# Kernel optimization log

Hardware: AMD Instinct MI355X
Metric: run time of the kernel (lower is better)

Reference implementation:

```python
import jax, jax.numpy as jnp
import numpy as np

B, L, D, H = 1, 1024, 768, 12
h = D // H  # 64
EPS = 1e-5
ALPHA = 0.01  # leaky relu slope


def setup_inputs() -> dict:
    key = jax.random.key(0)
    ks = jax.random.split(key, 10)
    s = 0.02
    f32 = jnp.float32
    return {
        "x": jax.random.normal(ks[0], (B, L, D), f32),
        "filters": jax.random.normal(ks[1], (L, h), f32) * s,  # spectral filters [L, h]
        "wq_w": jax.random.normal(ks[2], (D, D), f32) * s,
        "wq_b": jnp.zeros((D,), f32),
        "wk_w": jax.random.normal(ks[3], (D, D), f32) * s,
        "wk_b": jnp.zeros((D,), f32),
        "wv_w": jax.random.normal(ks[4], (D, D), f32) * s,
        "wv_b": jnp.zeros((D,), f32),
        "wo_w": jax.random.normal(ks[5], (D, D), f32) * s,
        "wo_b": jnp.zeros((D,), f32),
        "wg_w": jax.random.normal(ks[6], (h * h, 1), f32) * s,
        "wg_b": jnp.zeros((1,), f32),
        "qk_scale": jnp.ones((1, H, 1), f32) + jax.random.normal(ks[7], (1, H, 1), f32) * 0.02,
        "kv_scale": jnp.ones((1, H, 1, 1, 1), f32) + jax.random.normal(ks[8], (1, H, 1, 1, 1), f32) * 0.02,
    }


def _causal_fft_conv(f, u):
    """Per-head-channel causal FFT convolution. f: [L,h], u: [B,H,L,h] -> [B,H,L,h]."""
    n = 2 * L  # >= L + L - 1 for linear (full) convolution
    Ff = jnp.fft.rfft(f, n=n, axis=0)            # [n//2+1, h]
    Uf = jnp.fft.rfft(u, n=n, axis=2)            # [B,H,n//2+1,h]
    y = jnp.fft.irfft(Uf * Ff[None, None], n=n, axis=2)
    return y[:, :, :L, :]


def _l2norm(t):
    # matches F.normalize(dim=-1): x / max(||x||, 1e-12)
    nrm = jnp.sqrt(jnp.sum(t * t, axis=-1, keepdims=True))
    return t / jnp.maximum(nrm, 1e-12)


def _combine(a, b):
    """Associative combine: (m, s, n, Z, g) running-max / exp-sum / exp-weighted-v / outer-product / gate-sum."""
    m_x, s_x, n_x, Z_x, g_x = a
    m_y, s_y, n_y, Z_y, g_y = b
    m = jnp.maximum(m_x, m_y)
    ex = jnp.exp(m_x - m)
    ey = jnp.exp(m_y - m)
    return (m,
            s_x * ex + s_y * ey,
            n_x * ex[..., None] + n_y * ey[..., None],
            Z_x + Z_y,
            g_x + g_y)


def reference(x, filters, wq_w, wq_b, wk_w, wk_b, wv_w, wv_b, wo_w, wo_b,
              wg_w, wg_b, qk_scale, kv_scale):
    # split heads: [B,H,L,h]
    bhld = x.reshape(B, L, H, h).transpose(0, 2, 1, 3)
    # spectral filtering (tensordot_conv): per-channel causal conv with filters
    xt = _causal_fft_conv(filters, bhld)                       # [B,H,L,h]
    xt = xt.transpose(0, 2, 1, 3).reshape(B, L, D)             # [B,L,D]

    q = (xt @ wq_w + wq_b).reshape(B, L, H, h).transpose(0, 2, 1, 3)
    k = (xt @ wk_w + wk_b).reshape(B, L, H, h).transpose(0, 2, 1, 3)
    v = (xt @ wv_w + wv_b).reshape(B, L, H, h).transpose(0, 2, 1, 3)
    q, k, v = _l2norm(q), _l2norm(k), _l2norm(v)

    sim = jnp.einsum('bhld,bhld->bhl', q, k) * qk_scale         # [B,H,L]
    # Z[b,h,s,p,n] = v[b,h,s,p] * k[b,h,s,n]
    Z = jnp.einsum('bhsn,bhsp->bhspn', k, v) * kv_scale         # [B,H,L,h,h]

    gate_logits = Z.reshape(B, H, L, h * h) @ wg_w + wg_b       # [B,H,L,1]
    gl = jnp.where(gate_logits > 0, gate_logits, ALPHA * gate_logits)
    gates = (gl * gl + EPS)[..., 0]                             # [B,H,L]
    gated_Z = Z * gates[..., None, None]

    leaves = (sim, jnp.ones_like(sim), v, gated_Z, gates)
    m_s, s_s, n_s, Z_s, g_s = jax.lax.associative_scan(_combine, leaves, axis=2)

    linear_attn = n_s / (s_s[..., None] + EPS)                  # [B,H,L,h]
    softmax_w = jnp.exp(sim - m_s) / (s_s + EPS)                # [B,H,L]
    Hm = Z_s / (g_s[..., None, None] + EPS)                     # [B,H,L,h,h]
    ctx = jnp.einsum('bhtp,bhtpn->bhtn', q, Hm)                 # [B,H,L,h]
    qla = linear_attn
    lerp = ctx + (qla - ctx) * softmax_w[..., None]

    y = lerp.transpose(0, 2, 1, 3).reshape(B, L, D)
    return y @ wo_w + wo_b
```

## Files before the change

kernel.cpp:

```cpp
#include <hip/hip_runtime.h>
#include <hip/hip_bf16.h>

constexpr int LS = 1024;
constexpr int DM = 768;
constexpr int NH = 12;
constexpr int HD = 64;
constexpr float EPSF = 1e-5f;
constexpr float ALPHAF = 0.01f;

constexpr int SG = 16;
constexpr int NTL = LS / SG;
constexpr int WSZ = DM * DM;
constexpr int NPAR = 8;

typedef unsigned short u16;
typedef __attribute__((ext_vector_type(8))) short bf16x8;
typedef __attribute__((ext_vector_type(8))) unsigned short u16x8;
typedef __attribute__((ext_vector_type(4))) float f32x4;

__device__ __forceinline__ u16 f2b(float f) {
  unsigned u = __float_as_uint(f);
  u += 0x7FFFu + ((u >> 16) & 1u);
  return (u16)(u >> 16);
}
__device__ __forceinline__ float b2f(u16 b) {
  return __uint_as_float((unsigned)b << 16);
}

__device__ __forceinline__ void gld16(const u16* g, void* l) {
  __builtin_amdgcn_global_load_lds(
      (const __attribute__((address_space(1))) void*)g,
      (__attribute__((address_space(3))) void*)l, 16, 0, 0);
}

__global__ __launch_bounds__(256) void conv_txw_kernel(
    const float* __restrict__ x, const float* __restrict__ f,
    const float* __restrict__ wq, const float* __restrict__ wk,
    const float* __restrict__ wv, const float* __restrict__ wo,
    u16* __restrict__ wT, u16* __restrict__ pbase) {
  extern __shared__ char smem[];
  const int b = blockIdx.x;
  const int tid = threadIdx.x;

  if (b >= 1536) {
    const int b2 = b - 1536;
    const int kb = (b2 % 12) * 64, nb = ((b2 / 12) % 12) * 64, z = b2 / 144;
    const float* src = (z == 0) ? wq : (z == 1) ? wk : (z == 2) ? wv : wo;
    u16* dst = wT + (size_t)z * WSZ;
    float (*T)[65] = (float(*)[65])smem;
#pragma unroll
    for (int rep = 0; rep < 4; ++rep) {
      const int r = rep * 16 + (tid >> 4);
      const int c4 = (tid & 15) * 4;
      const float4 v4 = *(const float4*)(src + (size_t)(kb + r) * DM + nb + c4);
      T[r][c4] = v4.x; T[r][c4 + 1] = v4.y; T[r][c4 + 2] = v4.z; T[r][c4 + 3] = v4.w;
    }
    __syncthreads();
#pragma unroll
    for (int rep = 0; rep < 4; ++rep) {
      const int n = rep * 16 + (tid >> 4);
      const int k4 = (tid & 15) * 4;
      ushort4 o;
      o.x = f2b(T[k4 + 0][n]); o.y = f2b(T[k4 + 1][n]);
      o.z = f2b(T[k4 + 2][n]); o.w = f2b(T[k4 + 3][n]);
      *(ushort4*)(dst + (size_t)(nb + n) * DM + kb + k4) = o;
    }
    return;
  }

  const int lcg  = b & 15;
  const int head = (b >> 4) % 12;
  const int par  = b / 192;
  const int lane = tid & 63;
  const int wid  = tid >> 6;
  const int lc   = lcg * 4 + wid;
  const int l0   = lc * 16;

  const float* xg = x + head * HD + lane;
  const float* fg = f + lane;

  float acc[16];
#pragma unroll
  for (int t = 0; t < 16; ++t) acc[t] = 0.f;

  for (int sc = par; sc <= lc; sc += NPAR) {
    const int s0 = sc * 16;
    const int d0 = l0 - s0 - 15;
    float xw[16], fr[31];
#pragma unroll
    for (int m = 0; m < 16; ++m) xw[m] = xg[(s0 + m) * DM];
    if (sc < lc) {
#pragma unroll
      for (int m = 0; m < 31; ++m) fr[m] = fg[(d0 + m) * HD];
    } else {
#pragma unroll
      for (int m = 0; m < 15; ++m) fr[m] = 0.f;
#pragma unroll
      for (int m = 15; m < 31; ++m) fr[m] = fg[(d0 + m) * HD];
    }
#pragma unroll
    for (int li = 0; li < 16; ++li)
#pragma unroll
      for (int si = 0; si < 16; ++si)
        acc[li] = fmaf(fr[li - si + 15], xw[si], acc[li]);
  }

  u16* __restrict__ xt_p = pbase + (size_t)par * LS * DM;
#pragma unroll
  for (int li = 0; li < 16; ++li)
    xt_p[(size_t)(l0 + li) * DM + head * HD + lane] = f2b(acc[li]);
}

__global__ __launch_bounds__(256) void pack_xt(const u16* __restrict__ pbase,
                                               u16* __restrict__ xtb) {
  const size_t NT = (size_t)LS * DM;
  const size_t i = ((size_t)blockIdx.x * 256 + threadIdx.x) * 8;
  float s[8] = {};
#pragma unroll
  for (int p = 0; p < NPAR; ++p) {
    const u16x8 v8 = *(const u16x8*)(pbase + p * NT + i);
#pragma unroll
    for (int e = 0; e < 8; ++e) s[e] += b2f(v8[e]);
  }
  u16x8 o;
#pragma unroll
  for (int e = 0; e < 8; ++e) o[e] = f2b(s[e]);
  *(u16x8*)(xtb + i) = o;
}

__global__ __launch_bounds__(256) void qkv_mfma(const u16* __restrict__ xtb,
                                                const u16* __restrict__ wT,
                                                const float* __restrict__ bq,
                                                const float* __restrict__ bk,
                                                const float* __restrict__ bv,
                                                float* __restrict__ qo,
                                                float* __restrict__ ko,
                                                float* __restrict__ vo) {
  const int b = blockIdx.x;
  const int xcd = b & 7, j = b >> 3;
  const int rt = (xcd & 3) * 4 + j / 6;
  const int ct = (xcd >> 2) * 6 + j % 6;

  __shared__ u16 As[64 * 64];
  __shared__ u16 Bs[3][64 * 64];

  const int tid = threadIdx.x, w = tid >> 6, l = tid & 63;
  const int wr = w >> 1, wc = w & 1;

  const int srow1 = tid >> 3, sc16 = tid & 7;
  const int c16L1 = sc16 ^ (srow1 & 7);
  const int srow2 = srow1 + 32;
  const int c16L2 = sc16 ^ (srow2 & 7);

  const u16* Ag1 = xtb + (size_t)(rt * 64 + srow1) * DM + c16L1 * 8;
  const u16* Ag2 = xtb + (size_t)(rt * 64 + srow2) * DM + c16L2 * 8;

  char* lA = (char*)As + w * 1024;

  f32x4 acc[3][2][2] = {};
  for (int kb = 0; kb < DM; kb += 64) {
    gld16(Ag1 + kb, lA);
    gld16(Ag2 + kb, lA + 4096);
#pragma unroll
    for (int z = 0; z < 3; ++z) {
      const u16* wz = wT + (size_t)z * WSZ;
      const u16* Bg1 = wz + (size_t)(ct * 64 + srow1) * DM + c16L1 * 8;
      const u16* Bg2 = wz + (size_t)(ct * 64 + srow2) * DM + c16L2 * 8;
      char* lB = (char*)Bs[z] + w * 1024;
      gld16(Bg1 + kb, lB);
      gld16(Bg2 + kb, lB + 4096);
    }
    __syncthreads();
#pragma unroll
    for (int kk = 0; kk < 2; ++kk) {
      bf16x8 a[2];
#pragma unroll
      for (int ar = 0; ar < 2; ++ar) {
        const int row = wr * 32 + ar * 16 + (l & 15);
        const int c16 = ((kk << 2) + (l >> 4)) ^ (row & 7);
        a[ar] = *(const bf16x8*)((char*)As + row * 128 + c16 * 16);
      }
#pragma unroll
      for (int z = 0; z < 3; ++z) {
        bf16x8 bb[2];
#pragma unroll
        for (int bc = 0; bc < 2; ++bc) {
          const int col = wc * 32 + bc * 16 + (l & 15);
          const int c16 = ((kk << 2) + (l >> 4)) ^ (col & 7);
          bb[bc] = *(const bf16x8*)((char*)Bs[z] + col * 128 + c16 * 16);
        }
#pragma unroll
        for (int ar = 0; ar < 2; ++ar)
#pragma unroll
          for (int bc = 0; bc < 2; ++bc)
            acc[z][ar][bc] = __builtin_amdgcn_mfma_f32_16x16x32_bf16(
                a[ar], bb[bc], acc[z][ar][bc], 0, 0, 0);
      }
    }
    __syncthreads();
  }

  const float* biasArr[3] = {bq, bk, bv};
  float* outArr[3] = {qo, ko, vo};
  const int rbase = rt * 64 + wr * 32 + ((l >> 4) << 2);
  const int cb = wc * 32 + (l & 15);
#pragma unroll
  for (int z = 0; z < 3; ++z) {
    const float* bias = biasArr[z];
    float* out = outArr[z];
#pragma unroll
    for (int ar = 0; ar < 2; ++ar)
#pragma unroll
      for (int bc = 0; bc < 2; ++bc) {
        const int col = cb + bc * 16;
        const float bbv = bias[ct * 64 + col];
#pragma unroll
        for (int r = 0; r < 4; ++r)
          out[((size_t)ct * LS + rbase + ar * 16 + r) * HD + col] =
              acc[z][ar][bc][r] + bbv;
      }
  }
}

__global__ __launch_bounds__(256) void out_mfma(const u16* __restrict__ lerpb,
                                                const u16* __restrict__ woT,
                                                const float* __restrict__ bias,
                                                float* __restrict__ out) {
  const int b = blockIdx.x;
  const int xcd = b & 7, j = b >> 3;
  const int unit = xcd * 3 + (j >> 3), sub = j & 7;
  const int ct = unit >> 1, rt = (unit & 1) * 8 + sub;

  __shared__ u16 As[64 * 64];
  __shared__ u16 Bs[64 * 64];

  const int tid = threadIdx.x, w = tid >> 6, l = tid & 63;
  const int wr = w >> 1, wc = w & 1;

  const int srow1 = tid >> 3, sc16 = tid & 7;
  const int c16L1 = sc16 ^ (srow1 & 7);
  const int srow2 = srow1 + 32;
  const int c16L2 = sc16 ^ (srow2 & 7);

  const u16* Ag1 = lerpb + (size_t)(rt * 64 + srow1) * DM + c16L1 * 8;
  const u16* Ag2 = lerpb + (size_t)(rt * 64 + srow2) * DM + c16L2 * 8;
  const u16* Bg1 = woT + (size_t)(ct * 64 + srow1) * DM + c16L1 * 8;
  const u16* Bg2 = woT + (size_t)(ct * 64 + srow2) * DM + c16L2 * 8;

  char* lA = (char*)As + w * 1024;
  char* lB = (char*)Bs + w * 1024;

  f32x4 acc[2][2] = {};
  for (int kb = 0; kb < DM; kb += 64) {
    gld16(Ag1 + kb, lA);
    gld16(Ag2 + kb, lA + 4096);
    gld16(Bg1 + kb, lB);
    gld16(Bg2 + kb, lB + 4096);
    __syncthreads();
#pragma unroll
    for (int kk = 0; kk < 2; ++kk) {
      bf16x8 a[2], bb[2];
#pragma unroll
      for (int ar = 0; ar < 2; ++ar) {
        const int row = wr * 32 + ar * 16 + (l & 15);
        const int c16 = ((kk << 2) + (l >> 4)) ^ (row & 7);
        a[ar] = *(const bf16x8*)((char*)As + row * 128 + c16 * 16);
      }
#pragma unroll
      for (int bc = 0; bc < 2; ++bc) {
        const int col = wc * 32 + bc * 16 + (l & 15);
        const int c16 = ((kk << 2) + (l >> 4)) ^ (col & 7);
        bb[bc] = *(const bf16x8*)((char*)Bs + col * 128 + c16 * 16);
      }
#pragma unroll
      for (int ar = 0; ar < 2; ++ar)
#pragma unroll
        for (int bc = 0; bc < 2; ++bc)
          acc[ar][bc] = __builtin_amdgcn_mfma_f32_16x16x32_bf16(
              a[ar], bb[bc], acc[ar][bc], 0, 0, 0);
    }
    __syncthreads();
  }

  const int rbase = rt * 64 + wr * 32 + ((l >> 4) << 2);
  const int cb = wc * 32 + (l & 15);
#pragma unroll
  for (int ar = 0; ar < 2; ++ar)
#pragma unroll
    for (int bc = 0; bc < 2; ++bc) {
      const int col = ct * 64 + cb + bc * 16;
      const float bbv = bias[col];
#pragma unroll
      for (int r = 0; r < 4; ++r)
        out[(size_t)(rbase + ar * 16 + r) * DM + col] = acc[ar][bc][r] + bbv;
    }
}

__global__ __launch_bounds__(256) void nsg_state_kernel(
    float* __restrict__ q, float* __restrict__ k, float* __restrict__ v,
    const float* __restrict__ wg, const float* __restrict__ wgb,
    const float* __restrict__ qk_scale, const float* __restrict__ kv_scale,
    float* __restrict__ sim, float* __restrict__ gates,
    float* __restrict__ states, float* __restrict__ nes) {
  const int j = blockIdx.x, head = blockIdx.y;
  const int s0 = j * SG;
  const int tid = threadIdx.x;
  const int wid = tid >> 6, lane = tid & 63;
  __shared__ alignas(16) float Vs[SG][68];
  __shared__ alignas(16) float Kg[SG][68];
  __shared__ float Es[SG];

  auto red = [](float x) {
#pragma unroll
    for (int o = 32; o; o >>= 1) x += __shfl_xor(x, o);
    return x;
  };

  const float qks = qk_scale[head], kvs = kv_scale[head], wb = wgb[0];
#pragma unroll
  for (int it = 0; it < 4; ++it) {
    const int rr = wid * 4 + it;
    const size_t idx = ((size_t)head * LS + s0 + rr) * HD + lane;
    float qv = q[idx], kv = k[idx], vv = v[idx];
    const float qn = fmaxf(sqrtf(red(qv * qv)), 1e-12f);
    const float kn = fmaxf(sqrtf(red(kv * kv)), 1e-12f);
    const float vn = fmaxf(sqrtf(red(vv * vv)), 1e-12f);
    qv /= qn; kv /= kn; vv /= vn;
    q[idx] = qv; k[idx] = kv; v[idx] = vv;
    const float s = red(qv * kv) * qks;
    Vs[rr][lane] = vv;
    float t = 0.f;
#pragma unroll 8
    for (int p = 0; p < 64; ++p) t = fmaf(Vs[rr][p], wg[p * 64 + lane], t);
    float gl = red(t * kv) * kvs + wb;
    gl = gl > 0.f ? gl : ALPHAF * gl;
    const float g = gl * gl + EPSF;
    Kg[rr][lane] = kv * g;
    if (lane == 0) {
      sim[head * LS + s0 + rr] = s;
      gates[head * LS + s0 + rr] = g;
      Es[rr] = expf(s);
    }
  }
  __syncthreads();

  const int p0 = (tid >> 4) * 4, n0 = (tid & 15) * 4;
  float acc[4][4] = {};
  for (int s = 0; s < SG; ++s) {
    const float4 ra = *(const float4*)&Vs[s][p0];
    const float4 rb = *(const float4*)&Kg[s][n0];
    const float av[4] = {ra.x, ra.y, ra.z, ra.w};
    const float bv[4] = {rb.x, rb.y, rb.z, rb.w};
#pragma unroll
    for (int i = 0; i < 4; ++i)
#pragma unroll
      for (int jj = 0; jj < 4; ++jj)
        acc[i][jj] = fmaf(av[i], bv[jj], acc[i][jj]);
  }
  float* Sout = states + (size_t)(head * NTL + j) * 4096;
#pragma unroll
  for (int i = 0; i < 4; ++i)
    *(float4*)&Sout[(p0 + i) * 64 + n0] =
        make_float4(acc[i][0], acc[i][1], acc[i][2], acc[i][3]);

  if (tid < HD) {
    float ne = 0.f;
#pragma unroll
    for (int s = 0; s < SG; ++s) ne = fmaf(Es[s], Vs[s][tid], ne);
    nes[(size_t)(head * NTL + j) * HD + tid] = ne;
  }
}

__global__ __launch_bounds__(1024) void scan_prefix_kernel(
    const float* __restrict__ sim, const float* __restrict__ gates,
    float* __restrict__ m_s, float* __restrict__ Sraw, float* __restrict__ g_s,
    float* __restrict__ states, float* __restrict__ nes) {
  const int head = blockIdx.x, chunk = blockIdx.y;
  const int tid = threadIdx.x, lane = tid & 63, wid = tid >> 6;

  if (chunk == 0) {
    __shared__ float wm[16], wS[16], wg2[16];
    const float sv = sim[head * LS + tid];
    float m = sv, S = expf(sv), g = gates[head * LS + tid];
#pragma unroll
    for (int off = 1; off < 64; off <<= 1) {
      const float pm = __shfl_up(m, off);
      const float pS = __shfl_up(S, off);
      const float pg = __shfl_up(g, off);
      if (lane >= off) { m = fmaxf(m, pm); S += pS; g += pg; }
    }
    if (lane == 63) { wm[wid] = m; wS[wid] = S; wg2[wid] = g; }
    __syncthreads();
    for (int w2 = 0; w2 < wid; ++w2) {
      m = fmaxf(m, wm[w2]); S += wS[w2]; g += wg2[w2];
    }
    m_s[head * LS + tid] = m;
    Sraw[head * LS + tid] = S;
    g_s[head * LS + tid] = g;

    if (tid < HD) {
      float a = 0.f;
      float* nb = nes + (size_t)head * NTL * HD + tid;
#pragma unroll 4
      for (int jj = 0; jj < NTL; ++jj) {
        float* p = nb + (size_t)jj * HD;
        const float t = *p;
        *p = a;
        a += t;
      }
    }
  }

  {
    float a = 0.f;
    float* base = states + (size_t)head * NTL * 4096 + chunk * 1024 + tid;
#pragma unroll 4
    for (int jj = 0; jj < NTL; ++jj) {
      float* p = base + (size_t)jj * 4096;
      const float t = *p;
      *p = a;
      a += t;
    }
  }
}

__global__ __launch_bounds__(256) void apply_kernel(const float* __restrict__ q,
                                                    const float* __restrict__ k,
                                                    const float* __restrict__ v,
                                                    const float* __restrict__ sim,
                                                    const float* __restrict__ gates,
                                                    const float* __restrict__ m_s,
                                                    const float* __restrict__ Sraw,
                                                    const float* __restrict__ g_s,
                                                    const float* __restrict__ states,
                                                    const float* __restrict__ nes,
                                                    const float* __restrict__ kv_scale,
                                                    u16* __restrict__ lerpb) {
  const int bt = blockIdx.x, head = blockIdx.y;
  const int t0 = bt * SG;
  const int tid = threadIdx.x;
  __shared__ alignas(16) float Ps[64][68];
  __shared__ alignas(16) float Qs[SG][68];
  __shared__ alignas(16) float Vs[SG][68];
  __shared__ alignas(16) float Ks[SG][68];
  __shared__ alignas(16) float NEp[64];
  __shared__ float Ag[SG][SG + 1];
  __shared__ float Es[SG], Gs[SG];

  const float* Pg = states + (size_t)(head * NTL + bt) * 4096;
#pragma unroll
  for (int rep = 0; rep < 4; ++rep) {
    const int lin = rep * 1024 + tid * 4;
    *(float4*)&Ps[lin >> 6][lin & 63] = *(const float4*)(Pg + lin);
  }
  {
    const int r = tid >> 4, c = (tid & 15) * 4;
    const size_t rowbase = ((size_t)head * LS + t0 + r) * HD;
    *(float4*)&Qs[r][c] = *(const float4*)(q + rowbase + c);
    *(float4*)&Ks[r][c] = *(const float4*)(k + rowbase + c);
    *(float4*)&Vs[r][c] = *(const float4*)(v + rowbase + c);
  }
  if (tid < SG) {
    Es[tid] = expf(sim[head * LS + t0 + tid]);
    Gs[tid] = gates[head * LS + t0 + tid];
  }
  if (tid < HD) NEp[tid] = nes[(size_t)(head * NTL + bt) * HD + tid];
  __syncthreads();

  {
    const int t = tid >> 4, s = tid & 15;
    float a = 0.f;
    if (s <= t) {
#pragma unroll
      for (int p = 0; p < 64; p += 4) {
        const float4 q4 = *(const float4*)&Qs[t][p];
        const float4 v4 = *(const float4*)&Vs[s][p];
        a = fmaf(q4.x, v4.x, a); a = fmaf(q4.y, v4.y, a);
        a = fmaf(q4.z, v4.z, a); a = fmaf(q4.w, v4.w, a);
      }
      a *= Gs[s];
    }
    Ag[t][s] = a;
  }
  __syncthreads();

  const int r = tid >> 4, c0 = (tid & 15) * 4;
  float4 O = make_float4(0.f, 0.f, 0.f, 0.f);
#pragma unroll 8
  for (int p = 0; p < 64; ++p) {
    const float qv = Qs[r][p];
    const float4 p4 = *(const float4*)&Ps[p][c0];
    O.x = fmaf(qv, p4.x, O.x); O.y = fmaf(qv, p4.y, O.y);
    O.z = fmaf(qv, p4.z, O.z); O.w = fmaf(qv, p4.w, O.w);
  }
  float4 Nn = *(const float4*)&NEp[c0];
  for (int s = 0; s <= r; ++s) {
    const float ag = Ag[r][s];
    const float es = Es[s];
    const float4 k4 = *(const float4*)&Ks[s][c0];
    const float4 v4 = *(const float4*)&Vs[s][c0];
    O.x = fmaf(ag, k4.x, O.x); O.y = fmaf(ag, k4.y, O.y);
    O.z = fmaf(ag, k4.z, O.z); O.w = fmaf(ag, k4.w, O.w);
    Nn.x = fmaf(es, v4.x, Nn.x); Nn.y = fmaf(es, v4.y, Nn.y);
    Nn.z = fmaf(es, v4.z, Nn.z); Nn.w = fmaf(es, v4.w, Nn.w);
  }

  const int t = t0 + r;
  const float m  = m_s[head * LS + t];
  const float em = expf(-m);
  const float ss = Sraw[head * LS + t] * em;
  const float inv = 1.f / (ss + EPSF);
  const float sw  = expf(sim[head * LS + t] - m) * inv;
  const float gi  = kv_scale[head] / (g_s[head * LS + t] + EPSF);
  const float ei  = em * inv;
  float rx, ry, rz, rw;
  { const float cx = O.x * gi, la = Nn.x * ei; rx = cx + (la - cx) * sw; }
  { const float cx = O.y * gi, la = Nn.y * ei; ry = cx + (la - cx) * sw; }
  { const float cx = O.z * gi, la = Nn.z * ei; rz = cx + (la - cx) * sw; }
  { const float cx = O.w * gi, la = Nn.w * ei; rw = cx + (la - cx) * sw; }
  ushort4 ob;
  ob.x = f2b(rx); ob.y = f2b(ry); ob.z = f2b(rz); ob.w = f2b(rw);
  *(ushort4*)&lerpb[(size_t)t * DM + head * HD + c0] = ob;
}

extern "C" void kernel_launch(void* const* d_in, const int* in_sizes, int n_in,
                              void* d_out, int out_size, void* d_ws, size_t ws_size,
                              hipStream_t stream) {
  (void)in_sizes; (void)n_in; (void)out_size; (void)ws_size;
  const float* x        = (const float*)d_in[0];
  const float* filters  = (const float*)d_in[1];
  const float* wq_w     = (const float*)d_in[2];
  const float* wq_b     = (const float*)d_in[3];
  const float* wk_w     = (const float*)d_in[4];
  const float* wk_b     = (const float*)d_in[5];
  const float* wv_w     = (const float*)d_in[6];
  const float* wv_b     = (const float*)d_in[7];
  const float* wo_w     = (const float*)d_in[8];
  const float* wo_b     = (const float*)d_in[9];
  const float* wg_w     = (const float*)d_in[10];
  const float* wg_b     = (const float*)d_in[11];
  const float* qk_scale = (const float*)d_in[12];
  const float* kv_scale = (const float*)d_in[13];

  float* ws = (float*)d_ws;
  const size_t NT = (size_t)LS * DM;
  float* q     = ws;
  float* k     = ws + NT;
  float* v     = ws + 2 * NT;
  float* sim   = ws + 3 * NT;
  float* gates = sim + NH * LS;
  float* m_s   = gates + NH * LS;
  float* Sraw  = m_s + NH * LS;
  float* g_s   = Sraw + NH * LS;
  float* states = g_s + NH * LS;
  float* nes    = states + (size_t)NH * NTL * 4096;
  u16*   xtb    = (u16*)(nes + (size_t)NH * NTL * HD);
  u16*   wT     = xtb + NT;
  u16*   lerpb  = wT + 4 * (size_t)WSZ;
  u16*   pbase  = lerpb + NT;

  conv_txw_kernel<<<dim3(2112), 256, 16640, stream>>>(
      x, filters, wq_w, wk_w, wv_w, wo_w, wT, pbase);
  pack_xt<<<dim3(NT / 2048), 256, 0, stream>>>(pbase, xtb);
  qkv_mfma<<<dim3(192), 256, 0, stream>>>(xtb, wT, wq_b, wk_b, wv_b, q, k, v);
  nsg_state_kernel<<<dim3(NTL, NH), 256, 0, stream>>>(
      q, k, v, wg_w, wg_b, qk_scale, kv_scale, sim, gates, states, nes);
  scan_prefix_kernel<<<dim3(NH, 4), 1024, 0, stream>>>(
      sim, gates, m_s, Sraw, g_s, states, nes);
  apply_kernel<<<dim3(NTL, NH), 256, 0, stream>>>(
      q, k, v, sim, gates, m_s, Sraw, g_s, states, nes, kv_scale, lerpb);
  out_mfma<<<dim3(192), 256, 0, stream>>>(
      lerpb, wT + 3 * (size_t)WSZ, wo_b, (float*)d_out);
}
```

Baseline: 103.1 us.

## Transpose x and filters into channel-major layout before causal convolution

A prep kernel now transposes x to [head*channel, L] and the filters to a zero-padded channel-major buffer, alongside the existing weight transpose to bf16. The convolution kernel then reads contiguous float4 vectors per lane instead of one strided scalar per row, and the padding removes the diagonal-tile branch. This trades an extra kernel launch and an extra pass over x through memory for fewer scattered loads in the convolution's inner loop. It also separates the weight transpose from the convolution launch, so the two no longer share one grid.

```diff
diff --git a/kernel.cpp b/kernel.cpp
--- a/kernel.cpp
+++ b/kernel.cpp
@@ -12,6 +12,7 @@
 constexpr int NTL = LS / SG;
 constexpr int WSZ = DM * DM;
 constexpr int NPAR = 8;
+constexpr int FTS = 1056;
 
 typedef unsigned short u16;
 typedef __attribute__((ext_vector_type(8))) short bf16x8;
@@ -33,41 +34,97 @@
       (__attribute__((address_space(3))) void*)l, 16, 0, 0);
 }
 
-__global__ __launch_bounds__(256) void conv_txw_kernel(
+__global__ __launch_bounds__(256) void prep_kernel(
     const float* __restrict__ x, const float* __restrict__ f,
     const float* __restrict__ wq, const float* __restrict__ wk,
     const float* __restrict__ wv, const float* __restrict__ wo,
-    u16* __restrict__ wT, u16* __restrict__ pbase) {
-  extern __shared__ char smem[];
+    u16* __restrict__ wT, float* __restrict__ xT, float* __restrict__ fT) {
+  __shared__ float T[64][65];
   const int b = blockIdx.x;
   const int tid = threadIdx.x;
 
-  if (b >= 1536) {
-    const int b2 = b - 1536;
-    const int kb = (b2 % 12) * 64, nb = ((b2 / 12) % 12) * 64, z = b2 / 144;
-    const float* src = (z == 0) ? wq : (z == 1) ? wk : (z == 2) ? wv : wo;
-    u16* dst = wT + (size_t)z * WSZ;
-    float (*T)[65] = (float(*)[65])smem;
+  if (b < 192) {
+    const int head = b / 16, l0 = (b % 16) * 64;
+    const int r = tid >> 2, c4 = (tid & 3) * 16;
 #pragma unroll
     for (int rep = 0; rep < 4; ++rep) {
-      const int r = rep * 16 + (tid >> 4);
-      const int c4 = (tid & 15) * 4;
-      const float4 v4 = *(const float4*)(src + (size_t)(kb + r) * DM + nb + c4);
-      T[r][c4] = v4.x; T[r][c4 + 1] = v4.y; T[r][c4 + 2] = v4.z; T[r][c4 + 3] = v4.w;
+      const int c = c4 + rep * 4;
+      const float4 v4 = *(const float4*)(x + (size_t)(l0 + r) * DM + head * HD + c);
+      T[r][c] = v4.x; T[r][c + 1] = v4.y; T[r][c + 2] = v4.z; T[r][c + 3] = v4.w;
     }
     __syncthreads();
+    const int ch = tid >> 2, l4 = (tid & 3) * 16;
+    float* dst = xT + ((size_t)head * HD + ch) * LS + l0;
 #pragma unroll
     for (int rep = 0; rep < 4; ++rep) {
-      const int n = rep * 16 + (tid >> 4);
-      const int k4 = (tid & 15) * 4;
-      ushort4 o;
-      o.x = f2b(T[k4 + 0][n]); o.y = f2b(T[k4 + 1][n]);
-      o.z = f2b(T[k4 + 2][n]); o.w = f2b(T[k4 + 3][n]);
-      *(ushort4*)(dst + (size_t)(nb + n) * DM + kb + k4) = o;
+      const int li = l4 + rep * 4;
+      float4 v4;
+      v4.x = T[li + 0][ch]; v4.y = T[li + 1][ch];
+      v4.z = T[li + 2][ch]; v4.w = T[li + 3][ch];
+      *(float4*)(dst + li) = v4;
     }
     return;
   }
-
+  if (b < 208) {
+    const int d0 = (b - 192) * 64;
+    const int r = tid >> 2, c4 = (tid & 3) * 16;
+#pragma unroll
+    for (int rep = 0; rep < 4; ++rep) {
+      const int c = c4 + rep * 4;
+      const float4 v4 = *(const float4*)(f + (size_t)(d0 + r) * HD + c);
+      T[r][c] = v4.x; T[r][c + 1] = v4.y; T[r][c + 2] = v4.z; T[r][c + 3] = v4.w;
+    }
+    __syncthreads();
+    const int ch = tid >> 2, d4 = (tid & 3) * 16;
+    float* dst = fT + (size_t)ch * FTS + 16 + d0;
+#pragma unroll
+    for (int rep = 0; rep < 4; ++rep) {
+      const int di = d4 + rep * 4;
+      float4 v4;
+      v4.x = T[di + 0][ch]; v4.y = T[di + 1][ch];
+      v4.z = T[di + 2][ch]; v4.w = T[di + 3][ch];
+      *(float4*)(dst + di) = v4;
+    }
+    if (b == 192) {
+#pragma unroll
+      for (int kk = 0; kk < 8; ++kk) {
+        const int idx = kk * 256 + tid;
+        const int ch2 = idx >> 5, pp = idx & 31;
+        const int p = (pp < 16) ? pp : 1040 + (pp - 16);
+        fT[(size_t)ch2 * FTS + p] = 0.f;
+      }
+    }
+    return;
+  }
+
+  const int b2 = b - 208;
+  const int kb = (b2 % 12) * 64, nb = ((b2 / 12) % 12) * 64, z = b2 / 144;
+  const float* src = (z == 0) ? wq : (z == 1) ? wk : (z == 2) ? wv : wo;
+  u16* dst = wT + (size_t)z * WSZ;
+#pragma unroll
+  for (int rep = 0; rep < 4; ++rep) {
+    const int r = rep * 16 + (tid >> 4);
+    const int c4 = (tid & 15) * 4;
+    const float4 v4 = *(const float4*)(src + (size_t)(kb + r) * DM + nb + c4);
+    T[r][c4] = v4.x; T[r][c4 + 1] = v4.y; T[r][c4 + 2] = v4.z; T[r][c4 + 3] = v4.w;
+  }
+  __syncthreads();
+#pragma unroll
+  for (int rep = 0; rep < 4; ++rep) {
+    const int n = rep * 16 + (tid >> 4);
+    const int k4 = (tid & 15) * 4;
+    ushort4 o;
+    o.x = f2b(T[k4 + 0][n]); o.y = f2b(T[k4 + 1][n]);
+    o.z = f2b(T[k4 + 2][n]); o.w = f2b(T[k4 + 3][n]);
+    *(ushort4*)(dst + (size_t)(nb + n) * DM + kb + k4) = o;
+  }
+}
+
+__global__ __launch_bounds__(256) void conv_kernel(const float* __restrict__ xT,
+                                                   const float* __restrict__ fT,
+                                                   u16* __restrict__ pbase) {
+  const int b = blockIdx.x;
+  const int tid = threadIdx.x;
   const int lcg  = b & 15;
   const int head = (b >> 4) % 12;
   const int par  = b / 192;
@@ -76,8 +133,8 @@
   const int lc   = lcg * 4 + wid;
   const int l0   = lc * 16;
 
-  const float* xg = x + head * HD + lane;
-  const float* fg = f + lane;
+  const float* xrow = xT + ((size_t)head * HD + lane) * LS;
+  const float* frow = fT + (size_t)lane * FTS;
 
   float acc[16];
 #pragma unroll
@@ -85,24 +142,19 @@
 
   for (int sc = par; sc <= lc; sc += NPAR) {
     const int s0 = sc * 16;
-    const int d0 = l0 - s0 - 15;
-    float xw[16], fr[31];
-#pragma unroll
-    for (int m = 0; m < 16; ++m) xw[m] = xg[(s0 + m) * DM];
-    if (sc < lc) {
-#pragma unroll
-      for (int m = 0; m < 31; ++m) fr[m] = fg[(d0 + m) * HD];
-    } else {
-#pragma unroll
-      for (int m = 0; m < 15; ++m) fr[m] = 0.f;
-#pragma unroll
-      for (int m = 15; m < 31; ++m) fr[m] = fg[(d0 + m) * HD];
-    }
+    const int a0 = l0 - s0;
+    float xw[16], fb[32];
+#pragma unroll
+    for (int m = 0; m < 4; ++m)
+      *(float4*)&xw[m * 4] = *(const float4*)(xrow + s0 + m * 4);
+#pragma unroll
+    for (int m = 0; m < 8; ++m)
+      *(float4*)&fb[m * 4] = *(const float4*)(frow + a0 + m * 4);
 #pragma unroll
     for (int li = 0; li < 16; ++li)
 #pragma unroll
       for (int si = 0; si < 16; ++si)
-        acc[li] = fmaf(fr[li - si + 15], xw[si], acc[li]);
+        acc[li] = fmaf(fb[li - si + 16], xw[si], acc[li]);
   }
 
   u16* __restrict__ xt_p = pbase + (size_t)par * LS * DM;
@@ -554,13 +606,16 @@
   float* g_s   = Sraw + NH * LS;
   float* states = g_s + NH * LS;
   float* nes    = states + (size_t)NH * NTL * 4096;
-  u16*   xtb    = (u16*)(nes + (size_t)NH * NTL * HD);
+  float* xT     = nes + (size_t)NH * NTL * HD;
+  float* fT     = xT + NT;
+  u16*   xtb    = (u16*)(fT + (size_t)HD * FTS);
   u16*   wT     = xtb + NT;
   u16*   lerpb  = wT + 4 * (size_t)WSZ;
   u16*   pbase  = lerpb + NT;
 
-  conv_txw_kernel<<<dim3(2112), 256, 16640, stream>>>(
-      x, filters, wq_w, wk_w, wv_w, wo_w, wT, pbase);
+  prep_kernel<<<dim3(784), 256, 0, stream>>>(
+      x, filters, wq_w, wk_w, wv_w, wo_w, wT, xT, fT);
+  conv_kernel<<<dim3(1536), 256, 0, stream>>>(xT, fT, pbase);
   pack_xt<<<dim3(NT / 2048), 256, 0, stream>>>(pbase, xtb);
   qkv_mfma<<<dim3(192), 256, 0, stream>>>(xtb, wT, wq_b, wk_b, wv_b, q, k, v);
   nsg_state_kernel<<<dim3(NTL, NH), 256, 0, stream>>>(
```

Result: slower. 198.9 us (+92.9%).

## Compute causal spectral convolution as Toeplitz bf16 MFMA GEMM instead of FMA loops

Applied to the files above, without the earlier changes.

Replaces the scalar FMA direct causal convolution, which was split across 8 partial buffers and then summed by a pack kernel, with a Toeplitz-matrix formulation on bf16 MFMA. A prep kernel transposes x per channel into bf16 and builds pre-swizzled Toeplitz filter fragments, alongside the existing weight transposes. The new conv kernel accumulates the lower-triangular blocks with MFMA and writes xtb directly, removing the partial buffers and the pack pass. It risks extra precision loss from bf16 inputs to the convolution and uneven per-block work from the triangular loop.

```diff
diff --git a/kernel.cpp b/kernel.cpp
--- a/kernel.cpp
+++ b/kernel.cpp
@@ -11,7 +11,6 @@
 constexpr int SG = 16;
 constexpr int NTL = LS / SG;
 constexpr int WSZ = DM * DM;
-constexpr int NPAR = 8;
 
 typedef unsigned short u16;
 typedef __attribute__((ext_vector_type(8))) short bf16x8;
@@ -23,109 +22,121 @@
   u += 0x7FFFu + ((u >> 16) & 1u);
   return (u16)(u >> 16);
 }
-__device__ __forceinline__ float b2f(u16 b) {
-  return __uint_as_float((unsigned)b << 16);
-}
-
-__device__ __forceinline__ void gld16(const u16* g, void* l) {
+
+__device__ __forceinline__ void gld16(const void* g, void* l) {
   __builtin_amdgcn_global_load_lds(
       (const __attribute__((address_space(1))) void*)g,
       (__attribute__((address_space(3))) void*)l, 16, 0, 0);
 }
 
-__global__ __launch_bounds__(256) void conv_txw_kernel(
+__global__ __launch_bounds__(256) void prep_kernel(
     const float* __restrict__ x, const float* __restrict__ f,
     const float* __restrict__ wq, const float* __restrict__ wk,
     const float* __restrict__ wv, const float* __restrict__ wo,
-    u16* __restrict__ wT, u16* __restrict__ pbase) {
-  extern __shared__ char smem[];
+    u16* __restrict__ wT, u16* __restrict__ xtcT, u16* __restrict__ Afrag) {
+  __shared__ float T[64][65];
   const int b = blockIdx.x;
   const int tid = threadIdx.x;
 
-  if (b >= 1536) {
-    const int b2 = b - 1536;
-    const int kb = (b2 % 12) * 64, nb = ((b2 / 12) % 12) * 64, z = b2 / 144;
-    const float* src = (z == 0) ? wq : (z == 1) ? wk : (z == 2) ? wv : wo;
-    u16* dst = wT + (size_t)z * WSZ;
-    float (*T)[65] = (float(*)[65])smem;
+  if (b < 192) {
+    const int h = b / 16, l0 = (b % 16) * 64;
+    const int r = tid >> 2, c4 = (tid & 3) * 16;
 #pragma unroll
     for (int rep = 0; rep < 4; ++rep) {
-      const int r = rep * 16 + (tid >> 4);
-      const int c4 = (tid & 15) * 4;
-      const float4 v4 = *(const float4*)(src + (size_t)(kb + r) * DM + nb + c4);
-      T[r][c4] = v4.x; T[r][c4 + 1] = v4.y; T[r][c4 + 2] = v4.z; T[r][c4 + 3] = v4.w;
+      const int cc = c4 + rep * 4;
+      const float4 v4 = *(const float4*)(x + (size_t)(l0 + r) * DM + h * HD + cc);
+      T[r][cc] = v4.x; T[r][cc + 1] = v4.y; T[r][cc + 2] = v4.z; T[r][cc + 3] = v4.w;
     }
     __syncthreads();
-#pragma unroll
-    for (int rep = 0; rep < 4; ++rep) {
-      const int n = rep * 16 + (tid >> 4);
-      const int k4 = (tid & 15) * 4;
-      ushort4 o;
-      o.x = f2b(T[k4 + 0][n]); o.y = f2b(T[k4 + 1][n]);
-      o.z = f2b(T[k4 + 2][n]); o.w = f2b(T[k4 + 3][n]);
-      *(ushort4*)(dst + (size_t)(nb + n) * DM + kb + k4) = o;
-    }
+    const int cc = tid & 63, qq = tid >> 6;
+    u16* dst = xtcT + ((size_t)cc * 16 + h) * 1024 + l0 + qq * 16;
+    u16x8 o0, o1;
+#pragma unroll
+    for (int e = 0; e < 8; ++e) {
+      o0[e] = f2b(T[qq * 16 + e][cc]);
+      o1[e] = f2b(T[qq * 16 + 8 + e][cc]);
+    }
+    *(u16x8*)dst = o0;
+    *(u16x8*)(dst + 8) = o1;
     return;
   }
-
-  const int lcg  = b & 15;
-  const int head = (b >> 4) % 12;
-  const int par  = b / 192;
-  const int lane = tid & 63;
-  const int wid  = tid >> 6;
-  const int lc   = lcg * 4 + wid;
-  const int l0   = lc * 16;
-
-  const float* xg = x + head * HD + lane;
-  const float* fg = f + lane;
-
-  float acc[16];
-#pragma unroll
-  for (int t = 0; t < 16; ++t) acc[t] = 0.f;
-
-  for (int sc = par; sc <= lc; sc += NPAR) {
-    const int s0 = sc * 16;
-    const int d0 = l0 - s0 - 15;
-    float xw[16], fr[31];
-#pragma unroll
-    for (int m = 0; m < 16; ++m) xw[m] = xg[(s0 + m) * DM];
-    if (sc < lc) {
-#pragma unroll
-      for (int m = 0; m < 31; ++m) fr[m] = fg[(d0 + m) * HD];
-    } else {
-#pragma unroll
-      for (int m = 0; m < 15; ++m) fr[m] = 0.f;
-#pragma unroll
-      for (int m = 15; m < 31; ++m) fr[m] = fg[(d0 + m) * HD];
-    }
-#pragma unroll
-    for (int li = 0; li < 16; ++li)
-#pragma unroll
-      for (int si = 0; si < 16; ++si)
-        acc[li] = fmaf(fr[li - si + 15], xw[si], acc[li]);
-  }
-
-  u16* __restrict__ xt_p = pbase + (size_t)par * LS * DM;
-#pragma unroll
-  for (int li = 0; li < 16; ++li)
-    xt_p[(size_t)(l0 + li) * DM + head * HD + lane] = f2b(acc[li]);
-}
-
-__global__ __launch_bounds__(256) void pack_xt(const u16* __restrict__ pbase,
-                                               u16* __restrict__ xtb) {
-  const size_t NT = (size_t)LS * DM;
-  const size_t i = ((size_t)blockIdx.x * 256 + threadIdx.x) * 8;
-  float s[8] = {};
-#pragma unroll
-  for (int p = 0; p < NPAR; ++p) {
-    const u16x8 v8 = *(const u16x8*)(pbase + p * NT + i);
-#pragma unroll
-    for (int e = 0; e < 8; ++e) s[e] += b2f(v8[e]);
-  }
-  u16x8 o;
-#pragma unroll
-  for (int e = 0; e < 8; ++e) o[e] = f2b(s[e]);
-  *(u16x8*)(xtb + i) = o;
+  if (b < 256) {
+    const int d16 = b - 192;
+    const int c = tid & 63, g = tid >> 6;
+    u16* dst = Afrag + ((size_t)c * 64 + d16) * 512 + g * 8;
+#pragma unroll
+    for (int i = 0; i < 16; ++i) {
+      u16x8 o;
+#pragma unroll
+      for (int kk = 0; kk < 8; ++kk) {
+        const int d = 16 * d16 + i - 8 * g - kk;
+        const int dc = d < 0 ? 0 : d;
+        o[kk] = (d >= 0) ? f2b(f[(size_t)dc * HD + c]) : (u16)0;
+      }
+      *(u16x8*)(dst + i * 32) = o;
+    }
+    return;
+  }
+
+  const int b2 = b - 256;
+  const int kb = (b2 % 12) * 64, nb = ((b2 / 12) % 12) * 64, z = b2 / 144;
+  const float* src = (z == 0) ? wq : (z == 1) ? wk : (z == 2) ? wv : wo;
+  u16* dst = wT + (size_t)z * WSZ;
+#pragma unroll
+  for (int rep = 0; rep < 4; ++rep) {
+    const int r = rep * 16 + (tid >> 4);
+    const int c4 = (tid & 15) * 4;
+    const float4 v4 = *(const float4*)(src + (size_t)(kb + r) * DM + nb + c4);
+    T[r][c4] = v4.x; T[r][c4 + 1] = v4.y; T[r][c4 + 2] = v4.z; T[r][c4 + 3] = v4.w;
+  }
+  __syncthreads();
+#pragma unroll
+  for (int rep = 0; rep < 4; ++rep) {
+    const int n = rep * 16 + (tid >> 4);
+    const int k4 = (tid & 15) * 4;
+    ushort4 o;
+    o.x = f2b(T[k4 + 0][n]); o.y = f2b(T[k4 + 1][n]);
+    o.z = f2b(T[k4 + 2][n]); o.w = f2b(T[k4 + 3][n]);
+    *(ushort4*)(dst + (size_t)(nb + n) * DM + kb + k4) = o;
+  }
+}
+
+__global__ __launch_bounds__(256) void conv_mfma(const u16* __restrict__ xtcT,
+                                                 const u16* __restrict__ Afrag,
+                                                 u16* __restrict__ xtb) {
+  const int b = blockIdx.x;
+  const int tid = threadIdx.x;
+  const int w = tid >> 6, l = tid & 63;
+  const int c = b >> 2;
+  const int ltg = (b & 3) * 4 + w;
+
+  const u16* Ab = Afrag + (size_t)c * 32768 + ((l & 15) * 4 + (l >> 4)) * 8;
+  const u16* Bb = xtcT + (size_t)c * 16384 + (l & 15) * 1024 + (l >> 4) * 8;
+
+  f32x4 acc[4] = {};
+  const int nks = 2 * ltg + 2;
+  for (int ks = 0; ks < nks; ++ks) {
+    const bf16x8 Bf = *(const bf16x8*)(Bb + 32 * ks);
+#pragma unroll
+    for (int m = 0; m < 4; ++m) {
+      const int d16 = 4 * ltg + m - 2 * ks;
+      if (d16 >= 0) {
+        const bf16x8 Af = *(const bf16x8*)(Ab + d16 * 512);
+        acc[m] = __builtin_amdgcn_mfma_f32_16x16x32_bf16(Af, Bf, acc[m], 0, 0, 0);
+      }
+    }
+  }
+
+  const int j = l & 15;
+  if (j < 12) {
+#pragma unroll
+    for (int m = 0; m < 4; ++m) {
+      const int row0 = (4 * ltg + m) * 16 + ((l >> 4) << 2);
+#pragma unroll
+      for (int r = 0; r < 4; ++r)
+        xtb[(size_t)(row0 + r) * DM + j * 64 + c] = f2b(acc[m][r]);
+    }
+  }
 }
 
 __global__ __launch_bounds__(256) void qkv_mfma(const u16* __restrict__ xtb,
@@ -557,11 +568,12 @@
   u16*   xtb    = (u16*)(nes + (size_t)NH * NTL * HD);
   u16*   wT     = xtb + NT;
   u16*   lerpb  = wT + 4 * (size_t)WSZ;
-  u16*   pbase  = lerpb + NT;
-
-  conv_txw_kernel<<<dim3(2112), 256, 16640, stream>>>(
-      x, filters, wq_w, wk_w, wv_w, wo_w, wT, pbase);
-  pack_xt<<<dim3(NT / 2048), 256, 0, stream>>>(pbase, xtb);
+  u16*   xtcT   = lerpb + NT;
+  u16*   Afrag  = xtcT + (size_t)64 * 16 * 1024;
+
+  prep_kernel<<<dim3(832), 256, 0, stream>>>(
+      x, filters, wq_w, wk_w, wv_w, wo_w, wT, xtcT, Afrag);
+  conv_mfma<<<dim3(256), 256, 0, stream>>>(xtcT, Afrag, xtb);
   qkv_mfma<<<dim3(192), 256, 0, stream>>>(xtb, wT, wq_b, wk_b, wv_b, q, k, v);
   nsg_state_kernel<<<dim3(NTL, NH), 256, 0, stream>>>(
       q, k, v, wg_w, wg_b, qk_scale, kv_scale, sim, gates, states, nes);
```

Result: slower. 124.7 us (+20.9%).
